# Kernel tuning notes

Hardware: AMD Instinct MI355X
Metric: run time of the kernel (lower is better)

Reference implementation:

```python
import jax, jax.numpy as jnp
import numpy as np

SAMPLE_RATE = 44100
MAX_DURATION = 5.0
IR_LEN = int(SAMPLE_RATE * MAX_DURATION)   # 220500 taps (~5 s reverb tail)
AUDIO_LEN = SAMPLE_RATE * 60               # 60 s of mono audio


def setup_inputs() -> dict:
    key = jax.random.key(0)
    k1, k2 = jax.random.split(key)
    audio = jax.random.normal(k1, (1, AUDIO_LEN), dtype=jnp.float32)
    ir = jax.random.normal(k2, (IR_LEN,), dtype=jnp.float32)  # learned impulse response parameter
    return {"audio": audio, "ir": ir}


def _fft_correlate_valid(audio, ir):
    """Valid cross-correlation of (audio zero-padded by M-1) with ir.

    Matches torch: pad audio with M-1 trailing zeros, then conv1d (which is
    cross-correlation) in 'valid' mode -> output length N. Computed via FFT
    (O(N log N)) instead of direct O(N*M) convolution; identical math up to
    floating-point rounding.
    """
    B, N = audio.shape
    M = ir.shape[0]
    full = (N + M - 1) + M - 1          # full linear conv length of padded signal
    nfft = 1 << int(np.ceil(np.log2(full)))
    # trailing zero-pad covers both the explicit M-1 padding and FFT padding
    x = jnp.pad(audio, ((0, 0), (0, nfft - N)))
    k = jnp.pad(ir[::-1], (0, nfft - M))  # flip kernel: conv(x, flip(ir)) == correlate(x, ir)
    y = jnp.fft.irfft(jnp.fft.rfft(x, axis=-1) * jnp.fft.rfft(k), n=nfft, axis=-1)
    # valid cross-correlation region of the padded signal: indices [M-1, M-1+N)
    return jax.lax.dynamic_slice_in_dim(y, M - 1, N, axis=-1)


def reference(audio, ir):
    y = _fft_correlate_valid(audio, ir)       # [1, N]
    return y / jnp.max(jnp.abs(y))            # global max-abs normalization
```

## Files before the change

kernel.cpp:

```cpp
#include <hip/hip_runtime.h>
#include <hip/hip_fp16.h>


#define L_FFT (1 << 20)
#define GSTRIDE 273
#define PSCALE (1.0f / 1048576.0f)

__device__ __forceinline__ float2 h2f(__half2 h) { return __half22float2(h); }
__device__ __forceinline__ __half2 f2h(float2 v) { return __floats2half2_rn(v.x, v.y); }

__device__ __forceinline__ float2 cmul(float2 a, float2 b) {
    return make_float2(a.x * b.x - a.y * b.y, a.x * b.y + a.y * b.x);
}

__device__ __forceinline__ void rad4(float2 a, float2 b, float2 c, float2 d,
                                     float2& o0, float2& o1, float2& o2, float2& o3) {
    float2 apc = make_float2(a.x + c.x, a.y + c.y);
    float2 amc = make_float2(a.x - c.x, a.y - c.y);
    float2 bpd = make_float2(b.x + d.x, b.y + d.y);
    float2 bmd = make_float2(b.x - d.x, b.y - d.y);
    o0 = make_float2(apc.x + bpd.x, apc.y + bpd.y);
    o2 = make_float2(apc.x - bpd.x, apc.y - bpd.y);
    o1 = make_float2(amc.x + bmd.y, amc.y - bmd.x);
    o3 = make_float2(amc.x - bmd.y, amc.y + bmd.x);
}

__device__ __forceinline__ void dft16(float2 x[16]) {
    float2 tt[16];
    rad4(x[0], x[4], x[8],  x[12], tt[0],  tt[1],  tt[2],  tt[3]);
    rad4(x[1], x[5], x[9],  x[13], tt[4],  tt[5],  tt[6],  tt[7]);
    rad4(x[2], x[6], x[10], x[14], tt[8],  tt[9],  tt[10], tt[11]);
    rad4(x[3], x[7], x[11], x[15], tt[12], tt[13], tt[14], tt[15]);
    const float C1 = 0.92387953251128675613f, S1 = 0.38268343236508977173f;
    const float C2 = 0.70710678118654752440f;
    const float2 W1 = make_float2( C1, -S1);
    const float2 W2 = make_float2( C2, -C2);
    const float2 W3 = make_float2( S1, -C1);
    const float2 W6 = make_float2(-C2, -C2);
    const float2 W9 = make_float2(-C1,  S1);
    tt[5]  = cmul(tt[5],  W1);
    tt[6]  = cmul(tt[6],  W2);
    tt[7]  = cmul(tt[7],  W3);
    tt[9]  = cmul(tt[9],  W2);
    tt[10] = make_float2(tt[10].y, -tt[10].x);
    tt[11] = cmul(tt[11], W6);
    tt[13] = cmul(tt[13], W3);
    tt[14] = cmul(tt[14], W6);
    tt[15] = cmul(tt[15], W9);
    rad4(tt[0], tt[4], tt[8],  tt[12], x[0], x[4], x[8],  x[12]);
    rad4(tt[1], tt[5], tt[9],  tt[13], x[1], x[5], x[9],  x[13]);
    rad4(tt[2], tt[6], tt[10], tt[14], x[2], x[6], x[10], x[14]);
    rad4(tt[3], tt[7], tt[11], tt[15], x[3], x[7], x[11], x[15]);
}

__device__ __forceinline__ void fft256_core(float2 x[16], int i, int gi,
                                            float2* lds) {
    dft16(x);
    float sa, ca;
    __sincosf(-6.28318530717958647692f * (float)i * (1.0f / 256.0f), &sa, &ca);
    float2 w1 = make_float2(ca, sa);
    float2 w = w1;
#pragma unroll
    for (int k1 = 1; k1 < 16; ++k1) {
        x[k1] = cmul(x[k1], w);
        w = cmul(w, w1);
    }
    float2* base = lds + gi * GSTRIDE;
#pragma unroll
    for (int k1 = 0; k1 < 16; ++k1) base[i * 17 + k1] = x[k1];
    __syncthreads();
#pragma unroll
    for (int q1 = 0; q1 < 16; ++q1) x[q1] = base[q1 * 17 + i];
    dft16(x);
}

__device__ __forceinline__ void stage256_store(float2 x[16], __half2* db,
                                               int g, int i, int J, int log2J,
                                               float invLn) {
    int j = g & (J - 1);
    int np = g >> log2J;
    float base = -6.28318530717958647692f * (float)np * invLn;
    float sa, ca;
    __sincosf(base * (float)i, &sa, &ca);
    float2 w = make_float2(ca, sa);
    __sincosf(base * 16.0f, &sa, &ca);
    float2 w16 = make_float2(ca, sa);
    size_t ob = (size_t)256 * (g - j) + j;
#pragma unroll
    for (int k2 = 0; k2 < 16; ++k2) {
        db[ob + (size_t)(i + 16 * k2) * J] = f2h(cmul(x[k2], w));
        w = cmul(w, w16);
    }
}

__device__ __forceinline__ void store_j1_coalesced(float2 x[16], __half2* db,
                                                   int bx, int gi, int i, int tid,
                                                   float2* lds, float invL) {
    int g = bx * 16 + gi;
    float base = -6.28318530717958647692f * (float)g * invL;
    float sa, ca;
    __sincosf(base * (float)i, &sa, &ca);
    float2 w = make_float2(ca, sa);
    __sincosf(base * 16.0f, &sa, &ca);
    float2 w16 = make_float2(ca, sa);
    __syncthreads();
#pragma unroll
    for (int k2 = 0; k2 < 16; ++k2) {
        int e = 256 * gi + i + 16 * k2;
        lds[e + (e >> 8)] = cmul(x[k2], w);
        w = cmul(w, w16);
    }
    __syncthreads();
    __half2* dwin = db + (size_t)4096 * bx;
#pragma unroll
    for (int c = 0; c < 16; ++c) {
        int e2 = tid + 256 * c;
        dwin[e2] = f2h(lds[e2 + (e2 >> 8)]);
    }
}

__global__ void fwd1_pack(const float* __restrict__ audio,
                          const float* __restrict__ ir,
                          __half2* __restrict__ dst, int N, int M, int V) {
    __shared__ float2 lds[16 * GSTRIDE];
    int tid = threadIdx.x;
    int gi = tid & 15, i = tid >> 4;
    int bx = blockIdx.x, slot = blockIdx.y;
    int g = bx * 16 + gi;
    __half2* db = dst + (size_t)slot * L_FFT;

    float2 x[16];
#pragma unroll
    for (int q2 = 0; q2 < 16; ++q2) {
        int idx = g + (i + 16 * q2) * (L_FFT / 256);
        float2 v;
        if (slot == 0) {
            v = make_float2(audio[idx], audio[idx + V]);
        } else if (slot == 1) {
            float a2 = (idx + 2 * V < N) ? audio[idx + 2 * V] : 0.f;
            float a3 = (idx + 3 * V < N) ? audio[idx + 3 * V] : 0.f;
            v = make_float2(a2, a3);
        } else {
            v = make_float2((idx < M) ? ir[idx] : 0.f, 0.f);
        }
        x[q2] = v;
    }
    fft256_core(x, i, gi, lds);
    store_j1_coalesced(x, db, bx, gi, i, tid, lds, 1.0f / (float)L_FFT);
}

__global__ void inv1(const __half2* __restrict__ src, __half2* __restrict__ dst) {
    __shared__ float2 lds[16 * GSTRIDE];
    int tid = threadIdx.x;
    int gi = tid & 15, i = tid >> 4;
    int bx = blockIdx.x;
    int g = bx * 16 + gi;
    size_t boff = (size_t)blockIdx.y * L_FFT;
    const __half2* sb = src + boff;
    __half2* db = dst + boff;
    float2 x[16];
#pragma unroll
    for (int q2 = 0; q2 < 16; ++q2)
        x[q2] = h2f(sb[g + (i + 16 * q2) * (L_FFT / 256)]);
    fft256_core(x, i, gi, lds);
    store_j1_coalesced(x, db, bx, gi, i, tid, lds, 1.0f / (float)L_FFT);
}

__global__ void stage256(const __half2* __restrict__ src, __half2* __restrict__ dst,
                         int J, int log2J, float invLn) {
    __shared__ float2 lds[16 * GSTRIDE];
    int tid = threadIdx.x;
    int gi = tid & 15, i = tid >> 4;
    int g = blockIdx.x * 16 + gi;
    size_t boff = (size_t)blockIdx.y * L_FFT;
    const __half2* sb = src + boff;
    __half2* db = dst + boff;
    float2 x[16];
#pragma unroll
    for (int q2 = 0; q2 < 16; ++q2)
        x[q2] = h2f(sb[g + (i + 16 * q2) * (L_FFT / 256)]);
    fft256_core(x, i, gi, lds);
    stage256_store(x, db, g, i, J, log2J, invLn);
}

__global__ void fwd3_spectral(const __half2* __restrict__ A,
                              __half2* __restrict__ B) {
    __shared__ float2 XS[256 * 17];
    int tid = threadIdx.x;
    int p = blockIdx.y;
    int isFwd = (tid < 128);
    int j = isFwd ? tid : (tid - 128);
    int gf = blockIdx.x * 128 + j;
    int g = isFwd ? gf : ((65536 - gf) & 65535);
    int ptid = isFwd ? (tid + 128) : (tid - 128);

    float2 h[16];
#pragma unroll
    for (int q = 0; q < 16; ++q)
        h[q] = h2f(A[(size_t)2 * L_FFT + g + (size_t)q * 65536]);
    float2 x[16];
#pragma unroll
    for (int q = 0; q < 16; ++q)
        x[q] = h2f(A[(size_t)p * L_FFT + g + (size_t)q * 65536]);
    dft16(h);
    dft16(x);
#pragma unroll
    for (int r = 0; r < 16; ++r) XS[tid * 17 + r] = x[r];
    __syncthreads();
#pragma unroll
    for (int r = 0; r < 16; ++r) {
        int mi = (g == 0) ? ((16 - r) & 15) : (15 - r);
        float2 Z  = x[r];
        float2 Zr = XS[ptid * 17 + mi];
        float2 H  = h[r];
        float2 X0 = make_float2(0.5f * (Z.x + Zr.x), 0.5f * (Z.y - Zr.y));
        float2 X1 = make_float2(0.5f * (Z.y + Zr.y), 0.5f * (Zr.x - Z.x));
        float2 G0 = make_float2(X0.x * H.x + X0.y * H.y, X0.y * H.x - X0.x * H.y);
        float2 G1 = make_float2(X1.x * H.x + X1.y * H.y, X1.y * H.x - X1.x * H.y);
        B[(size_t)p * L_FFT + g + (size_t)r * 65536] =
            f2h(make_float2((G0.x - G1.y) * PSCALE,
                            -(G0.y + G1.x) * PSCALE));
    }
}

__global__ void inv3_max(const __half2* __restrict__ src,
                         float* __restrict__ partials, int N, int V) {
    int g = blockIdx.x * blockDim.x + threadIdx.x;
    int p = blockIdx.y;
    const __half2* sb = src + (size_t)p * L_FFT;
    float2 x[16];
#pragma unroll
    for (int q = 0; q < 16; ++q) x[q] = h2f(sb[g + q * 65536]);
    dft16(x);
    int lenO = (p == 1) ? (N - 3 * V) : V;
    float m = 0.f;
#pragma unroll
    for (int r = 0; r < 16; ++r) {
        int n = g + r * 65536;
        if (n < V)    m = fmaxf(m, fabsf(x[r].x));
        if (n < lenO) m = fmaxf(m, fabsf(x[r].y));
    }
    for (int o = 32; o > 0; o >>= 1) m = fmaxf(m, __shfl_xor(m, o));
    __shared__ float sm[4];
    int lane = threadIdx.x & 63, wv = threadIdx.x >> 6;
    if (lane == 0) sm[wv] = m;
    __syncthreads();
    if (threadIdx.x == 0)
        partials[blockIdx.y * gridDim.x + blockIdx.x] =
            fmaxf(fmaxf(sm[0], sm[1]), fmaxf(sm[2], sm[3]));
}

__global__ void norm_final(const __half2* __restrict__ src,
                           float* __restrict__ out,
                           const float* __restrict__ partials, int N, int V) {
    __shared__ float sm[4];
    int tid = threadIdx.x;
    int g = blockIdx.x * blockDim.x + tid;
    int p = blockIdx.y;
    const __half2* sb = src + (size_t)p * L_FFT;
    float2 x[16];
#pragma unroll
    for (int q = 0; q < 16; ++q) x[q] = h2f(sb[g + q * 65536]);

    float m = 0.f;
    for (int i = tid; i < 512; i += 256) m = fmaxf(m, partials[i]);
    for (int o = 32; o > 0; o >>= 1) m = fmaxf(m, __shfl_xor(m, o));
    int lane = tid & 63, wv = tid >> 6;
    if (lane == 0) sm[wv] = m;
    __syncthreads();
    float inv = 1.0f / fmaxf(fmaxf(sm[0], sm[1]), fmaxf(sm[2], sm[3]));

    dft16(x);
    int se = 2 * p, so = 2 * p + 1;
    int lenO = (p == 1) ? (N - 3 * V) : V;
#pragma unroll
    for (int r = 0; r < 16; ++r) {
        int n = g + r * 65536;
        if (n < V)    out[(size_t)se * V + n] = x[r].x * inv;
        if (n < lenO) out[(size_t)so * V + n] = -x[r].y * inv;
    }
}

extern "C" void kernel_launch(void* const* d_in, const int* in_sizes, int n_in,
                              void* d_out, int out_size, void* d_ws, size_t ws_size,
                              hipStream_t stream) {
    const float* audio = (const float*)d_in[0];
    const float* ir    = (const float*)d_in[1];
    float* out = (float*)d_out;

    const int N = in_sizes[0];
    const int M = in_sizes[1];
    const int V = L_FFT - M + 1;

    __half2* A = (__half2*)d_ws;
    __half2* B = A + (size_t)3 * L_FFT;
    float* partials = (float*)(B + (size_t)3 * L_FFT);

    const float invLn2 = 1.0f / 4096.0f;

    fwd1_pack<<<dim3(256, 3), 256, 0, stream>>>(audio, ir, B, N, M, V);
    stage256<<<dim3(256, 3), 256, 0, stream>>>(B, A, 256, 8, invLn2);
    fwd3_spectral<<<dim3(257, 2), 256, 0, stream>>>(A, B);
    inv1<<<dim3(256, 2), 256, 0, stream>>>(B, A);
    stage256<<<dim3(256, 2), 256, 0, stream>>>(A, B, 256, 8, invLn2);
    inv3_max<<<dim3(256, 2), 256, 0, stream>>>(B, partials, N, V);
    norm_final<<<dim3(256, 2), 256, 0, stream>>>(B, out, partials, N, V);
}
```

Measured before the change: 119.6 us.

## Fuse spectral multiply into first inverse FFT stage and drop real/imag split

The standalone spectral kernel and the first inverse 256-point stage are merged into one kernel. That kernel loads the forward spectra of the audio and the IR, applies the final radix-16 DFT, multiplies by the conjugated filter spectrum, then runs the inverse 256-point pass in registers and LDS. Because the filter is real, the packed complex audio spectrum can be multiplied directly by its spectrum, so the conjugate-symmetric split and recombine (and its LDS exchange) is removed. This saves a kernel launch and a full half-precision round trip through global memory. In exchange, the IR spectrum is now read by every audio plane in the fused kernel, and correctness depends on the conjugation convention matching the inverse transform.

New measurement: 117.6 us. No clear change (-1.6%).

```diff
diff --git a/kernel.cpp b/kernel.cpp
--- a/kernel.cpp
+++ b/kernel.cpp
@@ -149,23 +149,6 @@
     store_j1_coalesced(x, db, bx, gi, i, tid, lds, 1.0f / (float)L_FFT);
 }
 
-__global__ void inv1(const __half2* __restrict__ src, __half2* __restrict__ dst) {
-    __shared__ float2 lds[16 * GSTRIDE];
-    int tid = threadIdx.x;
-    int gi = tid & 15, i = tid >> 4;
-    int bx = blockIdx.x;
-    int g = bx * 16 + gi;
-    size_t boff = (size_t)blockIdx.y * L_FFT;
-    const __half2* sb = src + boff;
-    __half2* db = dst + boff;
-    float2 x[16];
-#pragma unroll
-    for (int q2 = 0; q2 < 16; ++q2)
-        x[q2] = h2f(sb[g + (i + 16 * q2) * (L_FFT / 256)]);
-    fft256_core(x, i, gi, lds);
-    store_j1_coalesced(x, db, bx, gi, i, tid, lds, 1.0f / (float)L_FFT);
-}
-
 __global__ void stage256(const __half2* __restrict__ src, __half2* __restrict__ dst,
                          int J, int log2J, float invLn) {
     __shared__ float2 lds[16 * GSTRIDE];
@@ -183,44 +166,34 @@
     stage256_store(x, db, g, i, J, log2J, invLn);
 }
 
-__global__ void fwd3_spectral(const __half2* __restrict__ A,
-                              __half2* __restrict__ B) {
-    __shared__ float2 XS[256 * 17];
-    int tid = threadIdx.x;
-    int p = blockIdx.y;
-    int isFwd = (tid < 128);
-    int j = isFwd ? tid : (tid - 128);
-    int gf = blockIdx.x * 128 + j;
-    int g = isFwd ? gf : ((65536 - gf) & 65535);
-    int ptid = isFwd ? (tid + 128) : (tid - 128);
-
-    float2 h[16];
-#pragma unroll
-    for (int q = 0; q < 16; ++q)
-        h[q] = h2f(A[(size_t)2 * L_FFT + g + (size_t)q * 65536]);
-    float2 x[16];
-#pragma unroll
-    for (int q = 0; q < 16; ++q)
-        x[q] = h2f(A[(size_t)p * L_FFT + g + (size_t)q * 65536]);
+__global__ void mid_spectral_inv1(const __half2* __restrict__ A,
+                                  __half2* __restrict__ B) {
+    __shared__ float2 lds[16 * GSTRIDE];
+    int tid = threadIdx.x;
+    int gi = tid & 15, i = tid >> 4;
+    int bx = blockIdx.x;
+    size_t boff = (size_t)blockIdx.y * L_FFT;
+    int g = bx * 16 + gi;
+    int gmid = g + (i << 12);
+
+    const __half2* sa = A + boff;
+    const __half2* sh = A + (size_t)2 * L_FFT;
+    float2 x[16], h[16];
+#pragma unroll
+    for (int q = 0; q < 16; ++q) {
+        x[q] = h2f(sa[gmid + (size_t)q * 65536]);
+        h[q] = h2f(sh[gmid + (size_t)q * 65536]);
+    }
+    dft16(x);
     dft16(h);
-    dft16(x);
-#pragma unroll
-    for (int r = 0; r < 16; ++r) XS[tid * 17 + r] = x[r];
-    __syncthreads();
 #pragma unroll
     for (int r = 0; r < 16; ++r) {
-        int mi = (g == 0) ? ((16 - r) & 15) : (15 - r);
-        float2 Z  = x[r];
-        float2 Zr = XS[ptid * 17 + mi];
-        float2 H  = h[r];
-        float2 X0 = make_float2(0.5f * (Z.x + Zr.x), 0.5f * (Z.y - Zr.y));
-        float2 X1 = make_float2(0.5f * (Z.y + Zr.y), 0.5f * (Zr.x - Z.x));
-        float2 G0 = make_float2(X0.x * H.x + X0.y * H.y, X0.y * H.x - X0.x * H.y);
-        float2 G1 = make_float2(X1.x * H.x + X1.y * H.y, X1.y * H.x - X1.x * H.y);
-        B[(size_t)p * L_FFT + g + (size_t)r * 65536] =
-            f2h(make_float2((G0.x - G1.y) * PSCALE,
-                            -(G0.y + G1.x) * PSCALE));
-    }
+        float2 Z = x[r], H = h[r];
+        x[r] = make_float2((Z.x * H.x + Z.y * H.y) * PSCALE,
+                           (Z.x * H.y - Z.y * H.x) * PSCALE);
+    }
+    fft256_core(x, i, gi, lds);
+    store_j1_coalesced(x, B + boff, bx, gi, i, tid, lds, 1.0f / (float)L_FFT);
 }
 
 __global__ void inv3_max(const __half2* __restrict__ src,
@@ -300,9 +273,8 @@
 
     fwd1_pack<<<dim3(256, 3), 256, 0, stream>>>(audio, ir, B, N, M, V);
     stage256<<<dim3(256, 3), 256, 0, stream>>>(B, A, 256, 8, invLn2);
-    fwd3_spectral<<<dim3(257, 2), 256, 0, stream>>>(A, B);
-    inv1<<<dim3(256, 2), 256, 0, stream>>>(B, A);
-    stage256<<<dim3(256, 2), 256, 0, stream>>>(A, B, 256, 8, invLn2);
-    inv3_max<<<dim3(256, 2), 256, 0, stream>>>(B, partials, N, V);
-    norm_final<<<dim3(256, 2), 256, 0, stream>>>(B, out, partials, N, V);
-}
+    mid_spectral_inv1<<<dim3(256, 2), 256, 0, stream>>>(A, B);
+    stage256<<<dim3(256, 2), 256, 0, stream>>>(B, A, 256, 8, invLn2);
+    inv3_max<<<dim3(256, 2), 256, 0, stream>>>(A, partials, N, V);
+    norm_final<<<dim3(256, 2), 256, 0, stream>>>(A, out, partials, N, V);
+}
```
